# Kernel optimization log

Hardware: AMD Instinct MI355X
Metric: run time of the kernel (lower is better)

Reference implementation:

```python
import jax, jax.numpy as jnp
import numpy as np

N_NODES = 50000
N_EDGES = 800000
D_IN = 128
D_OUT = 128
BN_EPS = 1e-5


def setup_inputs() -> dict:
    key = jax.random.key(0)
    ks = jax.random.split(key, 8)
    node_feats = jax.random.normal(ks[0], (N_NODES, D_IN), dtype=jnp.float32)
    src = jax.random.randint(ks[1], (N_EDGES,), 0, N_NODES, dtype=jnp.int32)
    dst = jax.random.randint(ks[2], (N_EDGES,), 0, N_NODES, dtype=jnp.int32)
    # Glorot-ish init for weights
    scale = 1.0 / np.sqrt(D_IN)
    W = jax.random.normal(ks[3], (D_IN, D_OUT), dtype=jnp.float32) * scale
    b = jnp.zeros((D_OUT,), dtype=jnp.float32)
    Wr = jax.random.normal(ks[4], (D_IN, D_OUT), dtype=jnp.float32) * scale
    br = jnp.zeros((D_OUT,), dtype=jnp.float32)
    gamma = jnp.ones((D_OUT,), dtype=jnp.float32)
    beta = jnp.zeros((D_OUT,), dtype=jnp.float32)
    return {"node_feats": node_feats, "src": src, "dst": dst, "W": W, "b": b,
            "Wr": Wr, "br": br, "gamma": gamma, "beta": beta}


def reference(node_feats, src, dst, W, b, Wr, br, gamma, beta):
    N = node_feats.shape[0]
    ones_e = jnp.ones(src.shape[0], dtype=node_feats.dtype)
    # DGL GraphConv norm='both': D_out^{-1/2} on source side, D_in^{-1/2} on dest side
    deg_out = jnp.clip(jax.ops.segment_sum(ones_e, src, num_segments=N), 1.0)
    deg_in = jnp.clip(jax.ops.segment_sum(ones_e, dst, num_segments=N), 1.0)
    h = node_feats * jax.lax.rsqrt(deg_out)[:, None]        # [N, D_in]
    agg = jax.ops.segment_sum(h[src], dst, num_segments=N)  # gather + scatter-add, [N, D_in]
    agg = agg * jax.lax.rsqrt(deg_in)[:, None]
    gcn = jax.nn.relu(agg @ W + b)                           # GraphConv activation=relu
    res = jax.nn.relu(node_feats @ Wr + br)                  # residual branch
    y = gcn + res
    # BatchNorm1d (training mode: biased batch stats)
    mean = jnp.mean(y, axis=0)
    var = jnp.mean(jnp.square(y - mean), axis=0)
    out = (y - mean) * jax.lax.rsqrt(var + BN_EPS) * gamma + beta
    return out
```

## Files before the change

### kernel.cpp

```cpp
#include <hip/hip_runtime.h>

#define N_NODES 50000
#define N_EDGES 800000
#define D 128
#define BN_EPS 1e-5f
#define AGG_BLOCKS 2048
#define CHUNKS 64
#define EPC (N_EDGES / CHUNKS)
#define EPC4 (EPC / 4)
#define HALF_BINS 25600
#define HALF_U32 12800
#define QUART_BINS 12800
#define QUART_U32 6400
#define NB_MERGE 100

typedef short bf16x8 __attribute__((ext_vector_type(8)));
typedef float f32x4  __attribute__((ext_vector_type(4)));
typedef float f32x2  __attribute__((ext_vector_type(2)));
typedef unsigned int u32x4 __attribute__((ext_vector_type(4)));
typedef int i32x4 __attribute__((ext_vector_type(4)));


__device__ __forceinline__ unsigned int pack_rne(float a, float b) {
    unsigned int ua = __float_as_uint(a); ua += 0x7fffu + ((ua >> 16) & 1u);
    unsigned int ub = __float_as_uint(b); ub += 0x7fffu + ((ub >> 16) & 1u);
    return (ua >> 16) | (ub & 0xffff0000u);
}
__device__ __forceinline__ unsigned short pack1_rne(float a) {
    unsigned int ua = __float_as_uint(a); ua += 0x7fffu + ((ua >> 16) & 1u);
    return (unsigned short)(ua >> 16);
}
__device__ __forceinline__ unsigned char pack1_fp8(float a) {
    unsigned int u = __builtin_amdgcn_cvt_pk_fp8_f32(a, a, 0, false);
    return (unsigned char)(u & 0xffu);
}

__device__ __forceinline__ void scan_blksum(const int* __restrict__ blk_sum,
                                            int* sh, int t) {
    int v = (t < NB_MERGE) ? blk_sum[t] : 0;
    if (t < 256) sh[t] = v;
    __syncthreads();
    int inc = v;
    #pragma unroll
    for (int off = 1; off < 256; off <<= 1) {
        int u = (t >= off && t < 256) ? sh[t - off] : 0;
        __syncthreads();
        inc += u;
        if (t < 256) sh[t] = inc;
        __syncthreads();
    }
}
#define BLK_OFF(sh, mb) ((mb) ? (sh)[(mb) - 1] : 0)

__global__ __launch_bounds__(256) void hist_kernel(
        const int* __restrict__ dst, const int* __restrict__ src,
        unsigned int* __restrict__ histD, unsigned int* __restrict__ histS,
        const float* __restrict__ W, const float* __restrict__ Wr,
        uint4* __restrict__ pW, uint4* __restrict__ pWr) {
    __shared__ unsigned int h[HALF_U32];
    int tid = threadIdx.x;
    int c = blockIdx.x, r = blockIdx.y;
    if (c >= CHUNKS) {
        if (r != 0 || blockIdx.z != 0) return;
        int t = (c - CHUNKS) * 256 + tid;
        const float* S = (t & 2048) ? Wr : W;
        uint4* Dst     = (t & 2048) ? pWr : pW;
        int e = t & 2047;
        int lane = e & 63, ks = (e >> 6) & 3, ct = e >> 8;
        int n  = ct * 16 + (lane & 15);
        int k0 = ks * 32 + (lane >> 4) * 8;
        float v[8];
        #pragma unroll
        for (int j = 0; j < 8; j++) v[j] = S[(k0 + j) * D + n];
        uint4 rr;
        rr.x = pack_rne(v[0], v[1]); rr.y = pack_rne(v[2], v[3]);
        rr.z = pack_rne(v[4], v[5]); rr.w = pack_rne(v[6], v[7]);
        Dst[e] = rr;
        return;
    }
    const int* keys = blockIdx.z ? src : dst;
    unsigned int* hist = blockIdx.z ? histS : histD;
    for (int j = tid; j < HALF_U32; j += 256) h[j] = 0u;
    __syncthreads();
    int lo = r * HALF_BINS;
    const i32x4* keys4 = (const i32x4*)(keys + c * EPC);
    for (int i = tid; i < EPC4; i += 256) {
        i32x4 k = __builtin_nontemporal_load(keys4 + i);
        int b0 = k.x - lo, b1 = k.y - lo, b2 = k.z - lo, b3 = k.w - lo;
        if ((unsigned)b0 < (unsigned)HALF_BINS) atomicAdd(&h[b0 >> 1], 1u << ((b0 & 1) * 16));
        if ((unsigned)b1 < (unsigned)HALF_BINS) atomicAdd(&h[b1 >> 1], 1u << ((b1 & 1) * 16));
        if ((unsigned)b2 < (unsigned)HALF_BINS) atomicAdd(&h[b2 >> 1], 1u << ((b2 & 1) * 16));
        if ((unsigned)b3 < (unsigned)HALF_BINS) atomicAdd(&h[b3 >> 1], 1u << ((b3 & 1) * 16));
    }
    __syncthreads();
    unsigned int* out = hist + ((size_t)(r * CHUNKS + c)) * HALF_U32;
    for (int j = tid; j < HALF_U32; j += 256) out[j] = h[j];
}

__global__ __launch_bounds__(256) void merge_kernel(
        unsigned int* __restrict__ histD, unsigned int* __restrict__ histS,
        int* __restrict__ cnt_in, int* __restrict__ cnt_out,
        int* __restrict__ row_ptr, int* __restrict__ blk_sum) {
    __shared__ int sh[256];
    int t = threadIdx.x;
    int bx = blockIdx.x;
    int r = bx / 50;
    int q = (bx % 50) * 256 + t;
    int n0 = r * HALF_BINS + q * 2;
    if (blockIdx.y) {
        size_t base = (size_t)r * CHUNKS * HALF_U32 + q;
        unsigned int vals[CHUNKS];
        #pragma unroll
        for (int c = 0; c < CHUNKS; c++)
            vals[c] = histS[base + (size_t)c * HALF_U32];
        unsigned int lo = 0, hi = 0;
        #pragma unroll
        for (int c = 0; c < CHUNKS; c++) {
            lo += vals[c] & 0xffffu; hi += vals[c] >> 16;
        }
        cnt_out[n0]     = (int)lo;
        cnt_out[n0 + 1] = (int)hi;
        return;
    }
    size_t base = (size_t)r * CHUNKS * HALF_U32 + q;
    unsigned int vals[CHUNKS];
    #pragma unroll
    for (int c = 0; c < CHUNKS; c++)
        vals[c] = histD[base + (size_t)c * HALF_U32];
    unsigned int lo = 0, hi = 0;
    #pragma unroll
    for (int c = 0; c < CHUNKS; c++) {
        unsigned int v = vals[c];
        histD[base + (size_t)c * HALF_U32] = lo | (hi << 16);
        lo += v & 0xffffu; hi += v >> 16;
    }
    cnt_in[n0]     = (int)lo;
    cnt_in[n0 + 1] = (int)hi;
    int pair = (int)lo + (int)hi;
    sh[t] = pair;
    __syncthreads();
    int inc = pair;
    #pragma unroll
    for (int off = 1; off < 256; off <<= 1) {
        int u = (t >= off) ? sh[t - off] : 0;
        __syncthreads();
        inc += u; sh[t] = inc;
        __syncthreads();
    }
    int excl = inc - pair;
    row_ptr[n0]     = excl;
    row_ptr[n0 + 1] = excl + (int)lo;
    if (t == 255) blk_sum[bx] = inc;
}

__global__ __launch_bounds__(512) void fill2_kernel(
        const int* __restrict__ src, const int* __restrict__ dst,
        const int* __restrict__ row_ptr, const unsigned int* __restrict__ histP,
        const int* __restrict__ blk_sum, int* __restrict__ csr_src) {
    __shared__ unsigned int h[QUART_U32];
    __shared__ int sho[256];
    int tid = threadIdx.x;
    scan_blksum(blk_sum, sho, tid);
    int c = blockIdx.x, s = blockIdx.y;
    int base = c * EPC;
    for (int j = tid; j < QUART_U32; j += 512) h[j] = 0u;
    __syncthreads();
    int lo = s * QUART_BINS;
    int r = s >> 1;
    const unsigned int* pre_c = histP + ((size_t)(r * CHUNKS + c)) * HALF_U32
                                      + (s & 1) * QUART_U32;
    for (int i = tid; i < EPC; i += 512) {
        int d = __builtin_nontemporal_load(dst + base + i);
        int b = d - lo;
        if ((unsigned)b < (unsigned)QUART_BINS) {
            int shft = (b & 1) * 16;
            unsigned int old = atomicAdd(&h[b >> 1], 1u << shft);
            unsigned int rank = (old >> shft) & 0xffffu;
            unsigned int pre = (pre_c[b >> 1] >> shft) & 0xffffu;
            int p = row_ptr[d] + BLK_OFF(sho, d >> 9) + (int)(pre + rank);
            csr_src[p] = __builtin_nontemporal_load(src + base + i);
        }
    }
}

__global__ __launch_bounds__(256) void gemm_mfma(
        const float* __restrict__ x, const uint4* __restrict__ pW,
        const uint4* __restrict__ pWr, const float* __restrict__ br,
        const unsigned int* __restrict__ cnt_out, unsigned char* __restrict__ hwb8,
        unsigned short* __restrict__ resb) {
    __shared__ unsigned short xs[64][136];
    int tid = threadIdx.x, wid = tid >> 6, lane = tid & 63;
    int quad = lane >> 4, l15 = lane & 15;
    int r0b = blockIdx.x * 64;
    const float4* xg = (const float4*)(x + (size_t)r0b * D);
    int maxidx = (N_NODES - r0b) * (D / 4);
    #pragma unroll
    for (int i = 0; i < 8; i++) {
        int idx = tid + 256 * i;
        float4 v = (idx < maxidx) ? xg[idx] : make_float4(0.f, 0.f, 0.f, 0.f);
        int row = idx >> 5, c0 = (idx & 31) * 4;
        *(unsigned int*)&xs[row][c0]     = pack_rne(v.x, v.y);
        *(unsigned int*)&xs[row][c0 + 2] = pack_rne(v.z, v.w);
    }
    __syncthreads();
    int wrow0 = wid * 16;
    bf16x8 A[4];
    #pragma unroll
    for (int ks = 0; ks < 4; ks++)
        A[ks] = *(const bf16x8*)&xs[wrow0 + l15][ks * 32 + quad * 8];
    f32x4 accW[8], accR[8];
    #pragma unroll
    for (int ct = 0; ct < 8; ct++) { accW[ct] = (f32x4)0.f; accR[ct] = (f32x4)0.f; }
    #pragma unroll
    for (int ct = 0; ct < 8; ct++) {
        #pragma unroll
        for (int ks = 0; ks < 4; ks++) {
            union { bf16x8 v; uint4 u; } Bw, Br2;
            Bw.u  = pW [(ct * 4 + ks) * 64 + lane];
            Br2.u = pWr[(ct * 4 + ks) * 64 + lane];
            accW[ct] = __builtin_amdgcn_mfma_f32_16x16x32_bf16(A[ks], Bw.v,  accW[ct], 0, 0, 0);
            accR[ct] = __builtin_amdgcn_mfma_f32_16x16x32_bf16(A[ks], Br2.v, accR[ct], 0, 0, 0);
        }
    }
    int r0 = r0b + wrow0;
    float ro[4]; int rowok[4];
    #pragma unroll
    for (int reg = 0; reg < 4; reg++) {
        int row = r0 + quad * 4 + reg;
        rowok[reg] = row < N_NODES;
        int cw = (int)cnt_out[rowok[reg] ? row : N_NODES - 1];
        ro[reg] = rsqrtf((float)(cw > 1 ? cw : 1));
    }
    #pragma unroll
    for (int ct = 0; ct < 8; ct++) {
        int c = ct * 16 + l15;
        float brv = br[c];
        #pragma unroll
        for (int reg = 0; reg < 4; reg++) {
            int row = r0 + quad * 4 + reg;
            if (rowok[reg]) {
                hwb8[(size_t)row * D + c] = pack1_fp8(accW[ct][reg] * ro[reg]);
                resb[(size_t)row * D + c] = pack1_rne(fmaxf(accR[ct][reg] + brv, 0.f));
            }
        }
    }
}

__device__ __forceinline__ float bf_lo(unsigned int v) { return __uint_as_float(v << 16); }
__device__ __forceinline__ float bf_hi(unsigned int v) { return __uint_as_float(v & 0xffff0000u); }

__device__ __forceinline__ void acc8f8(f32x2* a, const uint2 v) {
    a[0] += __builtin_amdgcn_cvt_pk_f32_fp8(v.x, false);
    a[1] += __builtin_amdgcn_cvt_pk_f32_fp8(v.x, true);
    a[2] += __builtin_amdgcn_cvt_pk_f32_fp8(v.y, false);
    a[3] += __builtin_amdgcn_cvt_pk_f32_fp8(v.y, true);
}
__device__ __forceinline__ void acc8f8m(f32x2* a, const uint2 v, float m) {
    f32x2 m2 = {m, m};
    a[0] += m2 * __builtin_amdgcn_cvt_pk_f32_fp8(v.x, false);
    a[1] += m2 * __builtin_amdgcn_cvt_pk_f32_fp8(v.x, true);
    a[2] += m2 * __builtin_amdgcn_cvt_pk_f32_fp8(v.y, false);
    a[3] += m2 * __builtin_amdgcn_cvt_pk_f32_fp8(v.y, true);
}

__device__ __forceinline__ void prefetch16(
        const unsigned char* __restrict__ hwb8, int myidx, int cnt,
        int qg, int ql,
        uint2& v0, uint2& v1, uint2& v2, uint2& v3,
        float& m0, float& m1, float& m2, float& m3) {
    int cm = cnt - 1; if (cm < 0) cm = 0;
    int j0 = qg,      j1 = 4 + qg, j2 = 8 + qg, j3 = 12 + qg;
    m0 = (j0 < cnt) ? 1.f : 0.f;
    m1 = (j1 < cnt) ? 1.f : 0.f;
    m2 = (j2 < cnt) ? 1.f : 0.f;
    m3 = (j3 < cnt) ? 1.f : 0.f;
    if (j0 > cm) j0 = cm;
    if (j1 > cm) j1 = cm;
    if (j2 > cm) j2 = cm;
    if (j3 > cm) j3 = cm;
    int p0 = __shfl(myidx, j0);
    int p1 = __shfl(myidx, j1);
    int p2 = __shfl(myidx, j2);
    int p3 = __shfl(myidx, j3);
    v0 = *((const uint2*)(hwb8 + (size_t)p0 * 128) + ql);
    v1 = *((const uint2*)(hwb8 + (size_t)p1 * 128) + ql);
    v2 = *((const uint2*)(hwb8 + (size_t)p2 * 128) + ql);
    v3 = *((const uint2*)(hwb8 + (size_t)p3 * 128) + ql);
}

__device__ __forceinline__ void gather_rest(
        const unsigned char* __restrict__ hwb8, int myidx, int cnt,
        int qg, int ql, f32x2* a) {
    int i = 16;
    for (; i + 16 <= cnt; i += 16) {
        int p0 = __shfl(myidx, i + qg);
        int p1 = __shfl(myidx, i + 4 + qg);
        int p2 = __shfl(myidx, i + 8 + qg);
        int p3 = __shfl(myidx, i + 12 + qg);
        uint2 v0 = *((const uint2*)(hwb8 + (size_t)p0 * 128) + ql);
        uint2 v1 = *((const uint2*)(hwb8 + (size_t)p1 * 128) + ql);
        uint2 v2 = *((const uint2*)(hwb8 + (size_t)p2 * 128) + ql);
        uint2 v3 = *((const uint2*)(hwb8 + (size_t)p3 * 128) + ql);
        acc8f8(a, v0); acc8f8(a, v1); acc8f8(a, v2); acc8f8(a, v3);
    }
    for (; i + 4 <= cnt; i += 4) {
        int p0 = __shfl(myidx, i + qg);
        uint2 v0 = *((const uint2*)(hwb8 + (size_t)p0 * 128) + ql);
        acc8f8(a, v0);
    }
    int t = cnt - i;
    if (t > 0) {
        int j = i + qg; if (j > cnt - 1) j = cnt - 1;
        int p0 = __shfl(myidx, j);
        uint2 v0 = *((const uint2*)(hwb8 + (size_t)p0 * 128) + ql);
        float m = (qg < t) ? 1.f : 0.f;
        acc8f8m(a, v0, m);
    }
}

__device__ __forceinline__ void gather_accum(
        const unsigned char* __restrict__ hwb8, int myidx, int cnt,
        int qg, int ql, f32x2* a) {
    int i = 0;
    for (; i + 16 <= cnt; i += 16) {
        int p0 = __shfl(myidx, i + qg);
        int p1 = __shfl(myidx, i + 4 + qg);
        int p2 = __shfl(myidx, i + 8 + qg);
        int p3 = __shfl(myidx, i + 12 + qg);
        uint2 v0 = *((const uint2*)(hwb8 + (size_t)p0 * 128) + ql);
        uint2 v1 = *((const uint2*)(hwb8 + (size_t)p1 * 128) + ql);
        uint2 v2 = *((const uint2*)(hwb8 + (size_t)p2 * 128) + ql);
        uint2 v3 = *((const uint2*)(hwb8 + (size_t)p3 * 128) + ql);
        acc8f8(a, v0); acc8f8(a, v1); acc8f8(a, v2); acc8f8(a, v3);
    }
    for (; i + 4 <= cnt; i += 4) {
        int p0 = __shfl(myidx, i + qg);
        uint2 v0 = *((const uint2*)(hwb8 + (size_t)p0 * 128) + ql);
        acc8f8(a, v0);
    }
    int t = cnt - i;
    if (t > 0) {
        int j = i + qg; if (j > cnt - 1) j = cnt - 1;
        int p0 = __shfl(myidx, j);
        uint2 v0 = *((const uint2*)(hwb8 + (size_t)p0 * 128) + ql);
        float m = (qg < t) ? 1.f : 0.f;
        acc8f8m(a, v0, m);
    }
}

__global__ __launch_bounds__(256) void agg_kernel(
        const unsigned char* __restrict__ hwb8, const int* __restrict__ row_ptr,
        const int* __restrict__ blk_sum, const unsigned int* __restrict__ cnt_in,
        const int* __restrict__ csr_src,
        const float* __restrict__ bias, const unsigned short* __restrict__ resb,
        unsigned short* __restrict__ yb, float* __restrict__ parts) {
    __shared__ float red[4 * 256];
    __shared__ int sho[256];
    int tid = threadIdx.x;
    scan_blksum(blk_sum, sho, tid);
    int lane = tid & 63, wid = tid >> 6;
    int wave = blockIdx.x * 4 + wid;
    int nw = AGG_BLOCKS * 4;
    int qg = lane >> 4;
    int ql = lane & 15;
    float s1[8] = {0,0,0,0,0,0,0,0}, s2[8] = {0,0,0,0,0,0,0,0};
    float4 bv0, bv1;
    if (lane < 16) {
        bv0 = ((const float4*)bias)[2 * lane];
        bv1 = ((const float4*)bias)[2 * lane + 1];
    }
    int e0_0 = 0, e1_0 = 0, mi_0 = 0; float ri_0 = 0.f; u32x4 rv_0 = (u32x4)0u;
    int e0_1 = 0, e1_1 = 0, mi_1 = 0; float ri_1 = 0.f; u32x4 rv_1 = (u32x4)0u;
    uint2 pv0, pv1, pv2, pv3; float pm0 = 0.f, pm1 = 0.f, pm2 = 0.f, pm3 = 0.f;
    pv0 = pv1 = pv2 = pv3 = make_uint2(0u, 0u);

    int n = wave;
    if (n < N_NODES) {
        e0_0 = row_ptr[n] + BLK_OFF(sho, n >> 9);
        e1_0 = row_ptr[n + 1] + BLK_OFF(sho, (n + 1) >> 9);
        int ci = (int)cnt_in[n];
        ri_0 = rsqrtf((float)(ci > 1 ? ci : 1));
        if (lane < 16) rv_0 = __builtin_nontemporal_load((const u32x4*)(resb + (size_t)n * D) + lane);
        int c0 = e1_0 - e0_0; if (c0 > 64) c0 = 64;
        mi_0 = (lane < c0) ? __builtin_nontemporal_load(csr_src + e0_0 + lane) : 0;
        prefetch16(hwb8, mi_0, c0, qg, ql, pv0, pv1, pv2, pv3, pm0, pm1, pm2, pm3);
    }
    int n1g = n + nw;
    if (n1g < N_NODES) {
        e0_1 = row_ptr[n1g] + BLK_OFF(sho, n1g >> 9);
        e1_1 = row_ptr[n1g + 1] + BLK_OFF(sho, (n1g + 1) >> 9);
        int ci = (int)cnt_in[n1g];
        ri_1 = rsqrtf((float)(ci > 1 ? ci : 1));
        if (lane < 16) rv_1 = __builtin_nontemporal_load((const u32x4*)(resb + (size_t)n1g * D) + lane);
        int c1 = e1_1 - e0_1; if (c1 > 64) c1 = 64;
        mi_1 = (lane < c1) ? __builtin_nontemporal_load(csr_src + e0_1 + lane) : 0;
    }

    while (n < N_NODES) {
        int n2 = n + 2 * nw;
        int e0_2 = 0, e1_2 = 0, mi_2 = 0; float ri_2 = 0.f; u32x4 rv_2 = (u32x4)0u;
        if (n2 < N_NODES) {
            e0_2 = row_ptr[n2] + BLK_OFF(sho, n2 >> 9);
            e1_2 = row_ptr[n2 + 1] + BLK_OFF(sho, (n2 + 1) >> 9);
            int ci = (int)cnt_in[n2];
            ri_2 = rsqrtf((float)(ci > 1 ? ci : 1));
            if (lane < 16) rv_2 = __builtin_nontemporal_load((const u32x4*)(resb + (size_t)n2 * D) + lane);
            int c2 = e1_2 - e0_2; if (c2 > 64) c2 = 64;
            mi_2 = (lane < c2) ? __builtin_nontemporal_load(csr_src + e0_2 + lane) : 0;
        }
        uint2 qv0, qv1, qv2, qv3; float qm0, qm1, qm2, qm3;
        {
            int c1 = e1_1 - e0_1; if (c1 > 64) c1 = 64;
            prefetch16(hwb8, mi_1, c1, qg, ql, qv0, qv1, qv2, qv3, qm0, qm1, qm2, qm3);
        }
        f32x2 av[4];
        av[0] = (f32x2)0.f; av[1] = (f32x2)0.f; av[2] = (f32x2)0.f; av[3] = (f32x2)0.f;
        acc8f8m(av, pv0, pm0); acc8f8m(av, pv1, pm1);
        acc8f8m(av, pv2, pm2); acc8f8m(av, pv3, pm3);
        {
            int cnt = e1_0 - e0_0; if (cnt > 64) cnt = 64;
            gather_rest(hwb8, mi_0, cnt, qg, ql, av);
        }
        for (int j0 = e0_0 + 64; j0 < e1_0; j0 += 64) {
            int cnt = e1_0 - j0; if (cnt > 64) cnt = 64;
            int mw = (lane < cnt) ? __builtin_nontemporal_load(csr_src + j0 + lane) : 0;
            gather_accum(hwb8, mw, cnt, qg, ql, av);
        }
        float a[8] = { av[0].x, av[0].y, av[1].x, av[1].y, av[2].x, av[2].y, av[3].x, av[3].y };
        #pragma unroll
        for (int k = 0; k < 8; k++) {
            a[k] += __shfl_xor(a[k], 16);
            a[k] += __shfl_xor(a[k], 32);
        }
        if (lane < 16) {
            float o[8];
            o[0] = fmaxf(a[0] * ri_0 + bv0.x, 0.f) + bf_lo(rv_0.x);
            o[1] = fmaxf(a[1] * ri_0 + bv0.y, 0.f) + bf_hi(rv_0.x);
            o[2] = fmaxf(a[2] * ri_0 + bv0.z, 0.f) + bf_lo(rv_0.y);
            o[3] = fmaxf(a[3] * ri_0 + bv0.w, 0.f) + bf_hi(rv_0.y);
            o[4] = fmaxf(a[4] * ri_0 + bv1.x, 0.f) + bf_lo(rv_0.z);
            o[5] = fmaxf(a[5] * ri_0 + bv1.y, 0.f) + bf_hi(rv_0.z);
            o[6] = fmaxf(a[6] * ri_0 + bv1.z, 0.f) + bf_lo(rv_0.w);
            o[7] = fmaxf(a[7] * ri_0 + bv1.w, 0.f) + bf_hi(rv_0.w);
            uint4 w;
            w.x = pack_rne(o[0], o[1]); w.y = pack_rne(o[2], o[3]);
            w.z = pack_rne(o[4], o[5]); w.w = pack_rne(o[6], o[7]);
            *((uint4*)(yb + (size_t)n * D) + lane) = w;
            #pragma unroll
            for (int k = 0; k < 8; k++) { s1[k] += o[k]; s2[k] += o[k] * o[k]; }
        }
        n += nw;
        e0_0 = e0_1; e1_0 = e1_1; mi_0 = mi_1; ri_0 = ri_1; rv_0 = rv_1;
        e0_1 = e0_2; e1_1 = e1_2; mi_1 = mi_2; ri_1 = ri_2; rv_1 = rv_2;
        pv0 = qv0; pv1 = qv1; pv2 = qv2; pv3 = qv3;
        pm0 = qm0; pm1 = qm1; pm2 = qm2; pm3 = qm3;
    }
    if (lane < 16) {
        int c0 = lane * 8;
        #pragma unroll
        for (int k = 0; k < 8; k++) {
            red[wid * 256 + c0 + k]       = s1[k];
            red[wid * 256 + 128 + c0 + k] = s2[k];
        }
    }
    __syncthreads();
    if (tid < 256) {
        float v = red[tid] + red[256 + tid] + red[512 + tid] + red[768 + tid];
        parts[(size_t)blockIdx.x * 256 + tid] = v;
    }
}

__global__ __launch_bounds__(256) void bn_fin2(
        const float* __restrict__ parts, const float* __restrict__ gamma,
        const float* __restrict__ beta, float* __restrict__ scsh) {
    __shared__ float rs1[256], rs2[256];
    int c = blockIdx.x, t = threadIdx.x;
    float s1 = 0.f, s2 = 0.f;
    for (int b = t; b < AGG_BLOCKS; b += 256) {
        s1 += parts[(size_t)b * 256 + c];
        s2 += parts[(size_t)b * 256 + 128 + c];
    }
    rs1[t] = s1; rs2[t] = s2;
    __syncthreads();
    for (int off = 128; off > 0; off >>= 1) {
        if (t < off) { rs1[t] += rs1[t + off]; rs2[t] += rs2[t + off]; }
        __syncthreads();
    }
    if (t == 0) {
        const float invN = 1.0f / (float)N_NODES;
        float mean = rs1[0] * invN;
        float var  = rs2[0] * invN - mean * mean;
        float sc = gamma[c] * rsqrtf(var + BN_EPS);
        scsh[c] = sc;
        scsh[128 + c] = beta[c] - mean * sc;
    }
}

__global__ void norm_kernel(const unsigned short* __restrict__ yb,
                            const float* __restrict__ scsh, float* __restrict__ out) {
    int i = blockIdx.x * blockDim.x + threadIdx.x;
    if (i < N_NODES * 16) {
        uint4 v = ((const uint4*)yb)[i];
        int c = (i & 15) * 8;
        f32x4 o0, o1;
        o0[0] = bf_lo(v.x) * scsh[c]     + scsh[128 + c];
        o0[1] = bf_hi(v.x) * scsh[c + 1] + scsh[128 + c + 1];
        o0[2] = bf_lo(v.y) * scsh[c + 2] + scsh[128 + c + 2];
        o0[3] = bf_hi(v.y) * scsh[c + 3] + scsh[128 + c + 3];
        o1[0] = bf_lo(v.z) * scsh[c + 4] + scsh[128 + c + 4];
        o1[1] = bf_hi(v.z) * scsh[c + 5] + scsh[128 + c + 5];
        o1[2] = bf_lo(v.w) * scsh[c + 6] + scsh[128 + c + 6];
        o1[3] = bf_hi(v.w) * scsh[c + 7] + scsh[128 + c + 7];
        f32x4* ov = (f32x4*)out + (size_t)i * 2;
        __builtin_nontemporal_store(o0, ov);
        __builtin_nontemporal_store(o1, ov + 1);
    }
}

extern "C" void kernel_launch(void* const* d_in, const int* in_sizes, int n_in,
                              void* d_out, int out_size, void* d_ws, size_t ws_size,
                              hipStream_t stream) {
    const float* x     = (const float*)d_in[0];
    const int*   src   = (const int*)d_in[1];
    const int*   dst   = (const int*)d_in[2];
    const float* W     = (const float*)d_in[3];
    const float* b     = (const float*)d_in[4];
    const float* Wr    = (const float*)d_in[5];
    const float* br    = (const float*)d_in[6];
    const float* gamma = (const float*)d_in[7];
    const float* beta  = (const float*)d_in[8];
    float* out = (float*)d_out;

    char* ws = (char*)d_ws;
    int*   cnt_in  = (int*)(ws + 0);
    int*   cnt_out = (int*)(ws + 262144);
    int*   row_ptr = (int*)(ws + 524288);
    float* scsh    = (float*)(ws + 1310720);
    int*   blk_sum = (int*)(ws + 1312768);
    int*   csr_src = (int*)(ws + 1576960);
    unsigned char*  hwb8 = (unsigned char*)(ws + 4800000);
    unsigned short* resb = (unsigned short*)(ws + 11200000);
    unsigned short* yb   = (unsigned short*)(ws + 24000000);
    float* parts   = (float*)(ws + 36800000);
    uint4* pW      = (uint4*)(ws + 38897152);
    uint4* pWr     = (uint4*)(ws + 38929920);
    unsigned int* histD = (unsigned int*)(ws + 38962688);
    unsigned int* histS = (unsigned int*)(ws + 45516288);

    hist_kernel<<<dim3(CHUNKS + 16, 2, 2), 256, 0, stream>>>(
        dst, src, histD, histS, W, Wr, pW, pWr);
    merge_kernel<<<dim3(NB_MERGE, 2), 256, 0, stream>>>(
        histD, histS, (int*)cnt_in, (int*)cnt_out, row_ptr, blk_sum);
    fill2_kernel<<<dim3(CHUNKS, 4), 512, 0, stream>>>(
        src, dst, row_ptr, histD, blk_sum, csr_src);
    gemm_mfma<<<(N_NODES + 63) / 64, 256, 0, stream>>>(
        x, pW, pWr, br, (const unsigned int*)cnt_out, hwb8, resb);
    agg_kernel<<<AGG_BLOCKS, 256, 0, stream>>>(
        hwb8, row_ptr, blk_sum, (const unsigned int*)cnt_in, csr_src, b, resb, yb, parts);
    bn_fin2<<<128, 256, 0, stream>>>(parts, gamma, beta, scsh);
    norm_kernel<<<(N_NODES * 16 + 255) / 256, 256, 0, stream>>>(yb, scsh, out);
}
```

Before: 211.9 us.

## Split histogram into quarter ranges and deepen aggregation gather prefetch to 32 edges

The histogram kernel now uses quarter-sized shared bins (12800) across four range blocks instead of two halves, halving LDS per block for higher occupancy, with merge and fill indexing adjusted to the new layout. The aggregation kernel prefetches 32 neighbor rows per node (8 loads per lane) in the software pipeline instead of 16, so more gather latency is hidden for the average degree of 16. The costs are more registers in the aggregation loop and twice as many key reads in the histogram pass.

```diff
diff --git a/kernel.cpp b/kernel.cpp
--- a/kernel.cpp
+++ b/kernel.cpp
@@ -8,11 +8,10 @@
 #define CHUNKS 64
 #define EPC (N_EDGES / CHUNKS)
 #define EPC4 (EPC / 4)
-#define HALF_BINS 25600
-#define HALF_U32 12800
 #define QUART_BINS 12800
 #define QUART_U32 6400
 #define NB_MERGE 100
+#define NB_PER_Q 25
 
 typedef short bf16x8 __attribute__((ext_vector_type(8)));
 typedef float f32x4  __attribute__((ext_vector_type(4)));
@@ -57,7 +56,7 @@
         unsigned int* __restrict__ histD, unsigned int* __restrict__ histS,
         const float* __restrict__ W, const float* __restrict__ Wr,
         uint4* __restrict__ pW, uint4* __restrict__ pWr) {
-    __shared__ unsigned int h[HALF_U32];
+    __shared__ unsigned int h[QUART_U32];
     int tid = threadIdx.x;
     int c = blockIdx.x, r = blockIdx.y;
     if (c >= CHUNKS) {
@@ -80,21 +79,21 @@
     }
     const int* keys = blockIdx.z ? src : dst;
     unsigned int* hist = blockIdx.z ? histS : histD;
-    for (int j = tid; j < HALF_U32; j += 256) h[j] = 0u;
-    __syncthreads();
-    int lo = r * HALF_BINS;
+    for (int j = tid; j < QUART_U32; j += 256) h[j] = 0u;
+    __syncthreads();
+    int lo = r * QUART_BINS;
     const i32x4* keys4 = (const i32x4*)(keys + c * EPC);
     for (int i = tid; i < EPC4; i += 256) {
         i32x4 k = __builtin_nontemporal_load(keys4 + i);
         int b0 = k.x - lo, b1 = k.y - lo, b2 = k.z - lo, b3 = k.w - lo;
-        if ((unsigned)b0 < (unsigned)HALF_BINS) atomicAdd(&h[b0 >> 1], 1u << ((b0 & 1) * 16));
-        if ((unsigned)b1 < (unsigned)HALF_BINS) atomicAdd(&h[b1 >> 1], 1u << ((b1 & 1) * 16));
-        if ((unsigned)b2 < (unsigned)HALF_BINS) atomicAdd(&h[b2 >> 1], 1u << ((b2 & 1) * 16));
-        if ((unsigned)b3 < (unsigned)HALF_BINS) atomicAdd(&h[b3 >> 1], 1u << ((b3 & 1) * 16));
-    }
-    __syncthreads();
-    unsigned int* out = hist + ((size_t)(r * CHUNKS + c)) * HALF_U32;
-    for (int j = tid; j < HALF_U32; j += 256) out[j] = h[j];
+        if ((unsigned)b0 < (unsigned)QUART_BINS) atomicAdd(&h[b0 >> 1], 1u << ((b0 & 1) * 16));
+        if ((unsigned)b1 < (unsigned)QUART_BINS) atomicAdd(&h[b1 >> 1], 1u << ((b1 & 1) * 16));
+        if ((unsigned)b2 < (unsigned)QUART_BINS) atomicAdd(&h[b2 >> 1], 1u << ((b2 & 1) * 16));
+        if ((unsigned)b3 < (unsigned)QUART_BINS) atomicAdd(&h[b3 >> 1], 1u << ((b3 & 1) * 16));
+    }
+    __syncthreads();
+    unsigned int* out = hist + ((size_t)(r * CHUNKS + c)) * QUART_U32;
+    for (int j = tid; j < QUART_U32; j += 256) out[j] = h[j];
 }
 
 __global__ __launch_bounds__(256) void merge_kernel(
@@ -104,15 +103,15 @@
     __shared__ int sh[256];
     int t = threadIdx.x;
     int bx = blockIdx.x;
-    int r = bx / 50;
-    int q = (bx % 50) * 256 + t;
-    int n0 = r * HALF_BINS + q * 2;
+    int r = bx / NB_PER_Q;
+    int q = (bx % NB_PER_Q) * 256 + t;
+    int n0 = bx * 512 + t * 2;
     if (blockIdx.y) {
-        size_t base = (size_t)r * CHUNKS * HALF_U32 + q;
+        size_t base = (size_t)r * CHUNKS * QUART_U32 + q;
         unsigned int vals[CHUNKS];
         #pragma unroll
         for (int c = 0; c < CHUNKS; c++)
-            vals[c] = histS[base + (size_t)c * HALF_U32];
+            vals[c] = histS[base + (size_t)c * QUART_U32];
         unsigned int lo = 0, hi = 0;
         #pragma unroll
         for (int c = 0; c < CHUNKS; c++) {
@@ -122,16 +121,16 @@
         cnt_out[n0 + 1] = (int)hi;
         return;
     }
-    size_t base = (size_t)r * CHUNKS * HALF_U32 + q;
+    size_t base = (size_t)r * CHUNKS * QUART_U32 + q;
     unsigned int vals[CHUNKS];
     #pragma unroll
     for (int c = 0; c < CHUNKS; c++)
-        vals[c] = histD[base + (size_t)c * HALF_U32];
+        vals[c] = histD[base + (size_t)c * QUART_U32];
     unsigned int lo = 0, hi = 0;
     #pragma unroll
     for (int c = 0; c < CHUNKS; c++) {
         unsigned int v = vals[c];
-        histD[base + (size_t)c * HALF_U32] = lo | (hi << 16);
+        histD[base + (size_t)c * QUART_U32] = lo | (hi << 16);
         lo += v & 0xffffu; hi += v >> 16;
     }
     cnt_in[n0]     = (int)lo;
@@ -166,9 +165,7 @@
     for (int j = tid; j < QUART_U32; j += 512) h[j] = 0u;
     __syncthreads();
     int lo = s * QUART_BINS;
-    int r = s >> 1;
-    const unsigned int* pre_c = histP + ((size_t)(r * CHUNKS + c)) * HALF_U32
-                                      + (s & 1) * QUART_U32;
+    const unsigned int* pre_c = histP + ((size_t)(s * CHUNKS + c)) * QUART_U32;
     for (int i = tid; i < EPC; i += 512) {
         int d = __builtin_nontemporal_load(dst + base + i);
         int b = d - lo;
@@ -263,35 +260,24 @@
     a[3] += m2 * __builtin_amdgcn_cvt_pk_f32_fp8(v.y, true);
 }
 
-__device__ __forceinline__ void prefetch16(
+__device__ __forceinline__ void prefetch32(
         const unsigned char* __restrict__ hwb8, int myidx, int cnt,
-        int qg, int ql,
-        uint2& v0, uint2& v1, uint2& v2, uint2& v3,
-        float& m0, float& m1, float& m2, float& m3) {
+        int qg, int ql, uint2* v, float* m) {
     int cm = cnt - 1; if (cm < 0) cm = 0;
-    int j0 = qg,      j1 = 4 + qg, j2 = 8 + qg, j3 = 12 + qg;
-    m0 = (j0 < cnt) ? 1.f : 0.f;
-    m1 = (j1 < cnt) ? 1.f : 0.f;
-    m2 = (j2 < cnt) ? 1.f : 0.f;
-    m3 = (j3 < cnt) ? 1.f : 0.f;
-    if (j0 > cm) j0 = cm;
-    if (j1 > cm) j1 = cm;
-    if (j2 > cm) j2 = cm;
-    if (j3 > cm) j3 = cm;
-    int p0 = __shfl(myidx, j0);
-    int p1 = __shfl(myidx, j1);
-    int p2 = __shfl(myidx, j2);
-    int p3 = __shfl(myidx, j3);
-    v0 = *((const uint2*)(hwb8 + (size_t)p0 * 128) + ql);
-    v1 = *((const uint2*)(hwb8 + (size_t)p1 * 128) + ql);
-    v2 = *((const uint2*)(hwb8 + (size_t)p2 * 128) + ql);
-    v3 = *((const uint2*)(hwb8 + (size_t)p3 * 128) + ql);
+    #pragma unroll
+    for (int i = 0; i < 8; i++) {
+        int j = i * 4 + qg;
+        m[i] = (j < cnt) ? 1.f : 0.f;
+        if (j > cm) j = cm;
+        int p = __shfl(myidx, j);
+        v[i] = *((const uint2*)(hwb8 + (size_t)p * 128) + ql);
+    }
 }
 
 __device__ __forceinline__ void gather_rest(
         const unsigned char* __restrict__ hwb8, int myidx, int cnt,
         int qg, int ql, f32x2* a) {
-    int i = 16;
+    int i = 32;
     for (; i + 16 <= cnt; i += 16) {
         int p0 = __shfl(myidx, i + qg);
         int p1 = __shfl(myidx, i + 4 + qg);
@@ -371,8 +357,9 @@
     }
     int e0_0 = 0, e1_0 = 0, mi_0 = 0; float ri_0 = 0.f; u32x4 rv_0 = (u32x4)0u;
     int e0_1 = 0, e1_1 = 0, mi_1 = 0; float ri_1 = 0.f; u32x4 rv_1 = (u32x4)0u;
-    uint2 pv0, pv1, pv2, pv3; float pm0 = 0.f, pm1 = 0.f, pm2 = 0.f, pm3 = 0.f;
-    pv0 = pv1 = pv2 = pv3 = make_uint2(0u, 0u);
+    uint2 pv[8]; float pm[8];
+    #pragma unroll
+    for (int i = 0; i < 8; i++) { pv[i] = make_uint2(0u, 0u); pm[i] = 0.f; }
 
     int n = wave;
     if (n < N_NODES) {
@@ -383,7 +370,7 @@
         if (lane < 16) rv_0 = __builtin_nontemporal_load((const u32x4*)(resb + (size_t)n * D) + lane);
         int c0 = e1_0 - e0_0; if (c0 > 64) c0 = 64;
         mi_0 = (lane < c0) ? __builtin_nontemporal_load(csr_src + e0_0 + lane) : 0;
-        prefetch16(hwb8, mi_0, c0, qg, ql, pv0, pv1, pv2, pv3, pm0, pm1, pm2, pm3);
+        prefetch32(hwb8, mi_0, c0, qg, ql, pv, pm);
     }
     int n1g = n + nw;
     if (n1g < N_NODES) {
@@ -408,15 +395,15 @@
             int c2 = e1_2 - e0_2; if (c2 > 64) c2 = 64;
             mi_2 = (lane < c2) ? __builtin_nontemporal_load(csr_src + e0_2 + lane) : 0;
         }
-        uint2 qv0, qv1, qv2, qv3; float qm0, qm1, qm2, qm3;
+        uint2 qv[8]; float qm[8];
         {
             int c1 = e1_1 - e0_1; if (c1 > 64) c1 = 64;
-            prefetch16(hwb8, mi_1, c1, qg, ql, qv0, qv1, qv2, qv3, qm0, qm1, qm2, qm3);
+            prefetch32(hwb8, mi_1, c1, qg, ql, qv, qm);
         }
         f32x2 av[4];
         av[0] = (f32x2)0.f; av[1] = (f32x2)0.f; av[2] = (f32x2)0.f; av[3] = (f32x2)0.f;
-        acc8f8m(av, pv0, pm0); acc8f8m(av, pv1, pm1);
-        acc8f8m(av, pv2, pm2); acc8f8m(av, pv3, pm3);
+        #pragma unroll
+        for (int i = 0; i < 8; i++) acc8f8m(av, pv[i], pm[i]);
         {
             int cnt = e1_0 - e0_0; if (cnt > 64) cnt = 64;
             gather_rest(hwb8, mi_0, cnt, qg, ql, av);
@@ -452,8 +439,8 @@
         n += nw;
         e0_0 = e0_1; e1_0 = e1_1; mi_0 = mi_1; ri_0 = ri_1; rv_0 = rv_1;
         e0_1 = e0_2; e1_1 = e1_2; mi_1 = mi_2; ri_1 = ri_2; rv_1 = rv_2;
-        pv0 = qv0; pv1 = qv1; pv2 = qv2; pv3 = qv3;
-        pm0 = qm0; pm1 = qm1; pm2 = qm2; pm3 = qm3;
+        #pragma unroll
+        for (int i = 0; i < 8; i++) { pv[i] = qv[i]; pm[i] = qm[i]; }
     }
     if (lane < 16) {
         int c0 = lane * 8;
@@ -547,7 +534,7 @@
     unsigned int* histD = (unsigned int*)(ws + 38962688);
     unsigned int* histS = (unsigned int*)(ws + 45516288);
 
-    hist_kernel<<<dim3(CHUNKS + 16, 2, 2), 256, 0, stream>>>(
+    hist_kernel<<<dim3(CHUNKS + 16, 4, 2), 256, 0, stream>>>(
         dst, src, histD, histS, W, Wr, pW, pWr);
     merge_kernel<<<dim3(NB_MERGE, 2), 256, 0, stream>>>(
         histD, histS, (int*)cnt_in, (int*)cnt_out, row_ptr, blk_sum);
```

Result: no change. 214.8 us (+1.4%).
